# Kernel tuning notes

Hardware: AMD Instinct MI355X
Metric: run time of the kernel (lower is better)

## Reference

```python
import jax, jax.numpy as jnp
import numpy as np

N = 8192
F = 128

def setup_inputs() -> dict:
    key = jax.random.key(0)
    k1, k2, k3 = jax.random.split(key, 3)
    x = jax.random.normal(k1, (N, F), dtype=jnp.float32)
    adj = jax.random.uniform(k2, (N, N), dtype=jnp.float32)
    # nn.Linear(2F, 1): weight [1, 2F] stored flat as [2F], bias scalar
    W = jax.random.normal(k3, (2 * F,), dtype=jnp.float32) * (1.0 / np.sqrt(2 * F))
    b = jnp.zeros((), dtype=jnp.float32)
    return {"x": x, "adj": adj, "W": W, "b": b}

def reference(x, adj, W, b):
    # Equivalent to cat([x_i, x_j]) @ W + b, without materializing [n, n, 2F]:
    # score[i, j] = x[i] @ W_left + x[j] @ W_right + b
    f = x.shape[1]
    w_left, w_right = W[:f], W[f:]
    s_left = x @ w_left    # [n]
    s_right = x @ w_right  # [n]
    att = jax.nn.sigmoid(s_left[:, None] + s_right[None, :] + b)  # [n, n]
    return adj * att
```

## Files before the change

### kernel.cpp

```cpp
#include <hip/hip_runtime.h>
#include <math.h>

#define NN 8192
#define FF 128

typedef float f32x4 __attribute__((ext_vector_type(4)));

__global__ __launch_bounds__(256) void compute_s_kernel(
    const float* __restrict__ x,
    const float* __restrict__ W,
    float* __restrict__ sL,
    float* __restrict__ sR)
{
    int gtid = blockIdx.x * blockDim.x + threadIdx.x;
    int row  = gtid >> 6;
    int lane = threadIdx.x & 63;
    if (row >= NN) return;

    const float2 xv = *reinterpret_cast<const float2*>(x + (size_t)row * FF + 2 * lane);
    const float2 wl = *reinterpret_cast<const float2*>(W + 2 * lane);
    const float2 wr = *reinterpret_cast<const float2*>(W + FF + 2 * lane);

    float accL = xv.x * wl.x + xv.y * wl.y;
    float accR = xv.x * wr.x + xv.y * wr.y;

    #pragma unroll
    for (int off = 32; off > 0; off >>= 1) {
        accL += __shfl_xor(accL, off, 64);
        accR += __shfl_xor(accR, off, 64);
    }
    if (lane == 0) {
        sL[row] = accL;
        sR[row] = accR;
    }
}

__device__ __forceinline__ float fast_sigmoid(float z) {
    return __builtin_amdgcn_rcpf(1.0f + __expf(-z));
}

__global__ __launch_bounds__(256) void dense_att_row_kernel(
    const float* __restrict__ adj,
    const float* __restrict__ sL,
    const float* __restrict__ sR,
    const float* __restrict__ bptr,
    float* __restrict__ out)
{
    const int row = blockIdx.x;
    const int tid = threadIdx.x;

    const f32x4* __restrict__ adjr = reinterpret_cast<const f32x4*>(adj) + (size_t)row * (NN / 4);
    const f32x4* __restrict__ sR4  = reinterpret_cast<const f32x4*>(sR);
    f32x4* __restrict__ outr       = reinterpret_cast<f32x4*>(out) + (size_t)row * (NN / 4);

    const float s = sL[row] + *bptr;

    f32x4 a[8], r[8];
    #pragma unroll
    for (int k = 0; k < 8; ++k) {
        a[k] = __builtin_nontemporal_load(&adjr[tid + 256 * k]);
    }
    #pragma unroll
    for (int k = 0; k < 8; ++k) {
        r[k] = sR4[tid + 256 * k];
    }

    #pragma unroll
    for (int k = 0; k < 8; ++k) {
        f32x4 o;
        o.x = a[k].x * fast_sigmoid(s + r[k].x);
        o.y = a[k].y * fast_sigmoid(s + r[k].y);
        o.z = a[k].z * fast_sigmoid(s + r[k].z);
        o.w = a[k].w * fast_sigmoid(s + r[k].w);
        __builtin_nontemporal_store(o, &outr[tid + 256 * k]);
    }
}

extern "C" void kernel_launch(void* const* d_in, const int* in_sizes, int n_in,
                              void* d_out, int out_size, void* d_ws, size_t ws_size,
                              hipStream_t stream) {
    const float* x   = (const float*)d_in[0];
    const float* adj = (const float*)d_in[1];
    const float* W   = (const float*)d_in[2];
    const float* b   = (const float*)d_in[3];
    float* out = (float*)d_out;

    float* sL = (float*)d_ws;
    float* sR = sL + NN;

    compute_s_kernel<<<NN / 4, 256, 0, stream>>>(x, W, sL, sR);
    dense_att_row_kernel<<<NN, 256, 0, stream>>>(adj, sL, sR, b, out);
}
```

Measured before the change: 97.21 us.

## Factor sigmoid exponent into per-row/col exps and process two rows per block

Rewrites the sigmoid as 1/(1+exp(-sL-b)*exp(-sR)), so the exponentials are computed once per row and column in the small kernel and the dense kernel needs only a multiply, add and reciprocal per element. The dense kernel now handles two rows per block and reuses the loaded expR vector across both. The aim is fewer transcendental ops and less redundant sR loading in a memory-bound kernel. The cost is higher register use per thread, and the product of two exps can overflow to inf, which still gives the correct limit of 0.

New measurement: 103.9 us. 1.07x slower.

```diff
diff --git a/kernel.cpp b/kernel.cpp
--- a/kernel.cpp
+++ b/kernel.cpp
@@ -9,8 +9,9 @@
 __global__ __launch_bounds__(256) void compute_s_kernel(
     const float* __restrict__ x,
     const float* __restrict__ W,
-    float* __restrict__ sL,
-    float* __restrict__ sR)
+    const float* __restrict__ bptr,
+    float* __restrict__ expL,
+    float* __restrict__ expR)
 {
     int gtid = blockIdx.x * blockDim.x + threadIdx.x;
     int row  = gtid >> 6;
@@ -30,49 +31,58 @@
         accR += __shfl_xor(accR, off, 64);
     }
     if (lane == 0) {
-        sL[row] = accL;
-        sR[row] = accR;
+        expL[row] = __expf(-(accL + *bptr));
+        expR[row] = __expf(-accR);
     }
 }
 
-__device__ __forceinline__ float fast_sigmoid(float z) {
-    return __builtin_amdgcn_rcpf(1.0f + __expf(-z));
-}
-
-__global__ __launch_bounds__(256) void dense_att_row_kernel(
+__global__ __launch_bounds__(256) void dense_att_row2_kernel(
     const float* __restrict__ adj,
-    const float* __restrict__ sL,
-    const float* __restrict__ sR,
-    const float* __restrict__ bptr,
+    const float* __restrict__ expL,
+    const float* __restrict__ expR,
     float* __restrict__ out)
 {
-    const int row = blockIdx.x;
-    const int tid = threadIdx.x;
+    const int row0 = blockIdx.x * 2;
+    const int row1 = row0 + 1;
+    const int tid  = threadIdx.x;
 
-    const f32x4* __restrict__ adjr = reinterpret_cast<const f32x4*>(adj) + (size_t)row * (NN / 4);
-    const f32x4* __restrict__ sR4  = reinterpret_cast<const f32x4*>(sR);
-    f32x4* __restrict__ outr       = reinterpret_cast<f32x4*>(out) + (size_t)row * (NN / 4);
+    const f32x4* __restrict__ adj0 = reinterpret_cast<const f32x4*>(adj) + (size_t)row0 * (NN / 4);
+    const f32x4* __restrict__ adj1 = reinterpret_cast<const f32x4*>(adj) + (size_t)row1 * (NN / 4);
+    const f32x4* __restrict__ eR4  = reinterpret_cast<const f32x4*>(expR);
+    f32x4* __restrict__ out0       = reinterpret_cast<f32x4*>(out) + (size_t)row0 * (NN / 4);
+    f32x4* __restrict__ out1       = reinterpret_cast<f32x4*>(out) + (size_t)row1 * (NN / 4);
 
-    const float s = sL[row] + *bptr;
+    const float eL0 = expL[row0];
+    const float eL1 = expL[row1];
 
-    f32x4 a[8], r[8];
+    f32x4 a0[8], a1[8], r[8];
     #pragma unroll
-    for (int k = 0; k < 8; ++k) {
-        a[k] = __builtin_nontemporal_load(&adjr[tid + 256 * k]);
-    }
+    for (int k = 0; k < 8; ++k)
+        a0[k] = __builtin_nontemporal_load(&adj0[tid + 256 * k]);
     #pragma unroll
-    for (int k = 0; k < 8; ++k) {
-        r[k] = sR4[tid + 256 * k];
-    }
+    for (int k = 0; k < 8; ++k)
+        a1[k] = __builtin_nontemporal_load(&adj1[tid + 256 * k]);
+    #pragma unroll
+    for (int k = 0; k < 8; ++k)
+        r[k] = eR4[tid + 256 * k];
 
     #pragma unroll
     for (int k = 0; k < 8; ++k) {
         f32x4 o;
-        o.x = a[k].x * fast_sigmoid(s + r[k].x);
-        o.y = a[k].y * fast_sigmoid(s + r[k].y);
-        o.z = a[k].z * fast_sigmoid(s + r[k].z);
-        o.w = a[k].w * fast_sigmoid(s + r[k].w);
-        __builtin_nontemporal_store(o, &outr[tid + 256 * k]);
+        o.x = a0[k].x * __builtin_amdgcn_rcpf(1.0f + eL0 * r[k].x);
+        o.y = a0[k].y * __builtin_amdgcn_rcpf(1.0f + eL0 * r[k].y);
+        o.z = a0[k].z * __builtin_amdgcn_rcpf(1.0f + eL0 * r[k].z);
+        o.w = a0[k].w * __builtin_amdgcn_rcpf(1.0f + eL0 * r[k].w);
+        __builtin_nontemporal_store(o, &out0[tid + 256 * k]);
+    }
+    #pragma unroll
+    for (int k = 0; k < 8; ++k) {
+        f32x4 o;
+        o.x = a1[k].x * __builtin_amdgcn_rcpf(1.0f + eL1 * r[k].x);
+        o.y = a1[k].y * __builtin_amdgcn_rcpf(1.0f + eL1 * r[k].y);
+        o.z = a1[k].z * __builtin_amdgcn_rcpf(1.0f + eL1 * r[k].z);
+        o.w = a1[k].w * __builtin_amdgcn_rcpf(1.0f + eL1 * r[k].w);
+        __builtin_nontemporal_store(o, &out1[tid + 256 * k]);
     }
 }
 
@@ -85,9 +95,9 @@
     const float* b   = (const float*)d_in[3];
     float* out = (float*)d_out;
 
-    float* sL = (float*)d_ws;
-    float* sR = sL + NN;
+    float* expL = (float*)d_ws;
+    float* expR = expL + NN;
 
-    compute_s_kernel<<<NN / 4, 256, 0, stream>>>(x, W, sL, sR);
-    dense_att_row_kernel<<<NN, 256, 0, stream>>>(adj, sL, sR, b, out);
+    compute_s_kernel<<<NN / 4, 256, 0, stream>>>(x, W, b, expL, expR);
+    dense_att_row2_kernel<<<NN / 2, 256, 0, stream>>>(adj, expL, expR, out);
 }
```
